# Kernel optimization log

Measured on AMD Instinct MI355X. Metric: run time of the kernel, lower is better.

The kernel has to match this reference:

```python
import jax, jax.numpy as jnp
import numpy as np

EMB = 64
D = 2 * EMB          # 128, feature dim of R / hidden of attention MLP
B, L = 128, 4096     # batch, sequence length
N_ITER = 50          # bisection iterations (entmax_bisect default)


def entmax_bisect(X, alpha, n_iter=N_ITER):
    """alpha-entmax via bisection over the last axis. X: [B, L], alpha: [B, 1] (>1)."""
    am1 = alpha - 1.0
    Xs = X * am1
    d = X.shape[-1]
    inv = 1.0 / am1
    max_val = jnp.max(Xs, axis=-1, keepdims=True)
    tau_lo0 = max_val - 1.0                       # gp(1, alpha) = 1
    tau_hi = max_val - (1.0 / d) ** am1           # gp(1/d, alpha)

    def p(tau):
        return jnp.clip(Xs - tau, 0.0, None) ** inv

    f_lo = jnp.sum(p(tau_lo0), axis=-1, keepdims=True) - 1.0

    def body(i, carry):
        tau_lo, dm, _ = carry
        dm = dm * 0.5
        tau_m = tau_lo + dm
        f_m = jnp.sum(p(tau_m), axis=-1, keepdims=True) - 1.0
        tau_lo = jnp.where(f_m * f_lo >= 0, tau_m, tau_lo)
        return (tau_lo, dm, tau_m)

    _, _, tau_m = jax.lax.fori_loop(0, n_iter, body, (tau_lo0, tau_hi - tau_lo0, tau_lo0))
    p_m = p(tau_m)
    return p_m / jnp.sum(p_m, axis=-1, keepdims=True)  # ensure_sum_one


def setup_inputs() -> dict:
    key = jax.random.key(0)
    ks = jax.random.split(key, 9)
    s = 1.0 / np.sqrt(D)
    R = jax.random.normal(ks[0], (B, L, D), dtype=jnp.float32)
    alpha = 1.25 + 0.5 * jax.random.uniform(ks[1], (B, 1), dtype=jnp.float32)  # in (1.25, 1.75)
    target = jax.random.normal(ks[2], (B, 1, D), dtype=jnp.float32)
    Wr1 = s * jax.random.normal(ks[3], (D, D), dtype=jnp.float32)      # Linear(2E, 2E), no bias
    Wr2 = s * jax.random.normal(ks[4], (D, EMB), dtype=jnp.float32)    # Linear(E, 2E) (shape-fixed), no bias
    Wr3 = s * jax.random.normal(ks[5], (1, D), dtype=jnp.float32)      # Linear(2E, 1), no bias
    bias_r = s * jax.random.normal(ks[6], (D,), dtype=jnp.float32)
    Wf_w = s * jax.random.normal(ks[7], (EMB, D), dtype=jnp.float32)   # Linear(2E, E)
    Wf_b = s * jax.random.normal(ks[8], (EMB,), dtype=jnp.float32)
    return {"R": R, "alpha": alpha, "target": target, "Wr1": Wr1, "Wr2": Wr2,
            "Wr3": Wr3, "bias_r": bias_r, "Wf_w": Wf_w, "Wf_b": Wf_b}


def reference(R, alpha, target, Wr1, Wr2, Wr3, bias_r, Wf_w, Wf_b):
    # q = Wf(target): [B, 1, E]
    q = jnp.einsum('btd,ed->bte', target, Wf_w) + Wf_b
    # additive attention score: Wr3 @ relu(Wr1 k + Wr2 q + b): [B, L]
    h = jax.nn.relu(jnp.einsum('bld,ed->ble', R, Wr1)
                    + jnp.einsum('bte,de->btd', q, Wr2)
                    + bias_r)
    scores = jnp.einsum('bld,d->bl', h, Wr3[0])
    # entmax sparsification over the sequence axis
    a = entmax_bisect(scores, alpha)
    # weighted sum of v = R: [B, D]
    res = jnp.einsum('bl,bld->bd', a, R)
    res = jax.nn.selu(res)
    res = res / jnp.linalg.norm(res, axis=-1, keepdims=True)
    return res
```

## Files before the change

kernel.cpp:

```cpp
#include <hip/hip_runtime.h>
#include <hip/hip_bf16.h>

#define B_ 128
#define L_ 4096
#define D_ 128
#define E_ 64

typedef __attribute__((ext_vector_type(8))) short short8;
typedef __attribute__((ext_vector_type(4))) float floatx4;

static __device__ __forceinline__ unsigned short f2bf(float x) {
  __hip_bfloat16 h = __float2bfloat16(x);
  union { __hip_bfloat16 h; unsigned short u; } c; c.h = h; return c.u;
}
static __device__ __forceinline__ float bf2f(unsigned short u) {
  union { unsigned short u; __hip_bfloat16 h; } c; c.u = u; return __bfloat162float(c.h);
}

__global__ __launch_bounds__(256) void prep(
    const float* __restrict__ Wr1, unsigned short* __restrict__ hi,
    unsigned short* __restrict__ lo, const float* __restrict__ target,
    const float* __restrict__ Wr2, const float* __restrict__ bias_r,
    const float* __restrict__ Wf_w, const float* __restrict__ Wf_b,
    float* __restrict__ cvec) {
  if (blockIdx.x < 64) {
    int t = blockIdx.x * 256 + threadIdx.x;
    int j = t & 7, lane = (t >> 3) & 63, ks = (t >> 9) & 3, nt = t >> 11;
    int e = nt * 16 + (lane & 15);
    int d = ks * 32 + (lane >> 4) * 8 + j;
    float x = Wr1[e * D_ + d];
    unsigned short h = f2bf(x);
    hi[t] = h;
    lo[t] = f2bf(x - bf2f(h));
  } else {
    const int sub = threadIdx.x >> 7;
    const int t = threadIdx.x & 127;
    const int b = (blockIdx.x - 64) * 2 + sub;
    __shared__ float tg[2][D_];
    __shared__ float q[2][E_];
    tg[sub][t] = target[b * D_ + t];
    __syncthreads();
    if (t < E_) {
      float s = Wf_b[t];
      #pragma unroll 8
      for (int d = 0; d < D_; ++d) s += tg[sub][d] * Wf_w[t * D_ + d];
      q[sub][t] = s;
    }
    __syncthreads();
    float s = bias_r[t];
    #pragma unroll 8
    for (int e = 0; e < E_; ++e) s += q[sub][e] * Wr2[t * E_ + e];
    cvec[b * D_ + t] = s;
  }
}

__global__ __launch_bounds__(256, 2) void pass_b(
    const float* __restrict__ R, const unsigned short* __restrict__ Whi,
    const unsigned short* __restrict__ Wlo, const float* __restrict__ cvec,
    const float* __restrict__ Wr3, float* __restrict__ scores) {
  __shared__ __align__(16) unsigned short sAhi[16384];
  __shared__ __align__(16) unsigned short sAlo[16384];
  const int b = blockIdx.x >> 5;
  const int lt = blockIdx.x & 31;
  const int t = threadIdx.x;
  const int wave = t >> 6, lane = t & 63;
  const int col = lane & 15, quad = lane >> 4;

  const float* Rbase = R + ((size_t)b * L_ + (size_t)lt * 128) * D_;
  #pragma unroll
  for (int i = 0; i < 8; ++i) {
    const int mt = wave * 2 + (i >> 2);
    const int ks = i & 3;
    const int row = mt * 16 + (lane & 15);
    const int c0 = ks * 32 + (lane >> 4) * 8;
    const float4* p = (const float4*)(Rbase + (size_t)row * D_ + c0);
    float4 v0 = p[0], v1 = p[1];
    float vv[8] = {v0.x, v0.y, v0.z, v0.w, v1.x, v1.y, v1.z, v1.w};
    union { unsigned short u[8]; short8 v; } H, Lo;
    #pragma unroll
    for (int j = 0; j < 8; ++j) {
      unsigned short h = f2bf(vv[j]);
      H.u[j] = h;
      Lo.u[j] = f2bf(vv[j] - bf2f(h));
    }
    const int base = ((mt * 4 + ks) * 64 + lane) * 8;
    *(short8*)(sAhi + base) = H.v;
    *(short8*)(sAlo + base) = Lo.v;
  }

  short8 bh[2][4], bl[2][4];
  #pragma unroll
  for (int n = 0; n < 2; ++n)
    #pragma unroll
    for (int ks = 0; ks < 4; ++ks) {
      int off = (((wave * 2 + n) * 4 + ks) * 64 + lane) * 8;
      bh[n][ks] = *(const short8*)(Whi + off);
      bl[n][ks] = *(const short8*)(Wlo + off);
    }

  floatx4 acc[8][2];
  #pragma unroll
  for (int mt = 0; mt < 8; ++mt)
    #pragma unroll
    for (int n = 0; n < 2; ++n) acc[mt][n] = (floatx4){0.f, 0.f, 0.f, 0.f};

  __syncthreads();

  #pragma unroll
  for (int mt = 0; mt < 8; ++mt) {
    #pragma unroll
    for (int ks = 0; ks < 4; ++ks) {
      int ai = ((mt * 4 + ks) * 64 + lane) * 8;
      short8 ah = *(const short8*)(sAhi + ai);
      short8 al = *(const short8*)(sAlo + ai);
      #pragma unroll
      for (int n = 0; n < 2; ++n) {
        acc[mt][n] = __builtin_amdgcn_mfma_f32_16x16x32_bf16(ah, bh[n][ks], acc[mt][n], 0, 0, 0);
        acc[mt][n] = __builtin_amdgcn_mfma_f32_16x16x32_bf16(al, bh[n][ks], acc[mt][n], 0, 0, 0);
        acc[mt][n] = __builtin_amdgcn_mfma_f32_16x16x32_bf16(ah, bl[n][ks], acc[mt][n], 0, 0, 0);
      }
    }
  }

  float w3[2], cb[2];
  #pragma unroll
  for (int n = 0; n < 2; ++n) {
    int e = (wave * 2 + n) * 16 + col;
    w3[n] = Wr3[e];
    cb[n] = cvec[b * D_ + e];
  }
  float part[8][4];
  #pragma unroll
  for (int mt = 0; mt < 8; ++mt)
    #pragma unroll
    for (int r = 0; r < 4; ++r) {
      float s = 0.f;
      #pragma unroll
      for (int n = 0; n < 2; ++n)
        s += w3[n] * fmaxf(acc[mt][n][r] + cb[n], 0.f);
      s += __shfl_xor(s, 1, 64);
      s += __shfl_xor(s, 2, 64);
      s += __shfl_xor(s, 4, 64);
      s += __shfl_xor(s, 8, 64);
      part[mt][r] = s;
    }
  __syncthreads();
  float* red = (float*)sAhi;
  if (col == 0) {
    #pragma unroll
    for (int mt = 0; mt < 8; ++mt)
      #pragma unroll
      for (int r = 0; r < 4; ++r)
        red[wave * 128 + mt * 16 + quad * 4 + r] = part[mt][r];
  }
  __syncthreads();
  if (t < 128) {
    float s = (red[t] + red[128 + t]) + (red[256 + t] + red[384 + t]);
    scores[(size_t)b * L_ + lt * 128 + t] = s;
  }
}

__global__ __launch_bounds__(512) void pass_cd(
    const float* __restrict__ scores, const float* __restrict__ alpha,
    const float* __restrict__ R, float* __restrict__ out) {
  const int b = blockIdx.x, t = threadIdx.x;
  const int wave = t >> 6, lane = t & 63;
  __shared__ float sX[L_];
  __shared__ unsigned short sI[L_];
  __shared__ float sW[L_];
  __shared__ unsigned short sJ[L_];
  __shared__ float ppart[512];
  __shared__ float sred[2][8];
  __shared__ int scnt, smcnt;
  const float am1 = alpha[b] - 1.0f;
  const float inv = 1.0f / am1;
  const float* S = scores + (size_t)b * L_;
  float Xs[8];
  #pragma unroll
  for (int i = 0; i < 8; ++i) Xs[i] = S[i * 512 + t] * am1;
  if (t == 0) { scnt = 0; smcnt = 0; }

  float mx = Xs[0];
  #pragma unroll
  for (int i = 1; i < 8; ++i) mx = fmaxf(mx, Xs[i]);
  #pragma unroll
  for (int m = 32; m >= 1; m >>= 1) mx = fmaxf(mx, __shfl_xor(mx, m, 64));
  if (lane == 0) sred[0][wave] = mx;
  __syncthreads();
  mx = sred[0][0];
  #pragma unroll
  for (int w = 1; w < 8; ++w) mx = fmaxf(mx, sred[0][w]);

  const float tau_lo0 = mx - 1.0f;
  #pragma unroll
  for (int i = 0; i < 8; ++i) {
    if (Xs[i] > tau_lo0) {
      int pos = atomicAdd(&scnt, 1);
      sX[pos] = Xs[i];
      sI[pos] = (unsigned short)(i * 512 + t);
    }
  }
  __syncthreads();
  const int n = scnt;

  float tau_lo = tau_lo0;
  float dm = (mx - exp2f(-12.0f * am1)) - tau_lo;

  int pc = 1;
  auto sumP = [&](float tau) -> float {
    const int par = pc & 1;
    ++pc;
    float s = 0.f;
    for (int k = t; k < n; k += 512) {
      float u = sX[k] - tau;
      if (u > 0.f) s += exp2f(inv * __log2f(u));
    }
    #pragma unroll
    for (int m = 32; m >= 1; m >>= 1) s += __shfl_xor(s, m, 64);
    if (lane == 0) sred[par][wave] = s;
    __syncthreads();
    float r = sred[par][0];
    #pragma unroll
    for (int w = 1; w < 8; ++w) r += sred[par][w];
    return r;
  };

  const float f_lo = sumP(tau_lo) - 1.0f;
  float tau_m = tau_lo;
  for (int it = 0; it < 40; ++it) {
    dm *= 0.5f;
    tau_m = tau_lo + dm;
    float f_m = sumP(tau_m) - 1.0f;
    if (f_m * f_lo >= 0.f) tau_lo = tau_m;
  }

  float s = 0.f;
  for (int k = t; k < n; k += 512) {
    float u = sX[k] - tau_m;
    if (u > 0.f) {
      float p = exp2f(inv * __log2f(u));
      s += p;
      int pos = atomicAdd(&smcnt, 1);
      sJ[pos] = sI[k];
      sW[pos] = p;
    }
  }
  {
    const int par = pc & 1;
    ++pc;
    #pragma unroll
    for (int m = 32; m >= 1; m >>= 1) s += __shfl_xor(s, m, 64);
    if (lane == 0) sred[par][wave] = s;
    __syncthreads();
    s = sred[par][0];
    #pragma unroll
    for (int w = 1; w < 8; ++w) s += sred[par][w];
  }
  const int ns = smcnt;
  const float rs = 1.0f / s;

  const float* Rb = R + (size_t)b * L_ * D_;
  const int g = t >> 7, c = t & 127;
  float acc = 0.f;
  int k = g;
  for (; k + 4 < ns; k += 8) {
    int i0 = sJ[k], i1 = sJ[k + 4];
    float w0 = sW[k], w1 = sW[k + 4];
    acc += w0 * Rb[(size_t)i0 * D_ + c] + w1 * Rb[(size_t)i1 * D_ + c];
  }
  for (; k < ns; k += 4) acc += sW[k] * Rb[(size_t)sJ[k] * D_ + c];
  __syncthreads();
  ppart[t] = acc;
  __syncthreads();
  float r = 0.f;
  if (t < 128) {
    float a2 = ((ppart[t] + ppart[t + 128]) + (ppart[t + 256] + ppart[t + 384])) * rs;
    const float sc = 1.0507009873554805f, al = 1.6732632423543772f;
    r = a2 > 0.f ? sc * a2 : sc * al * (expf(a2) - 1.0f);
  }
  float q = r * r;
  #pragma unroll
  for (int m = 32; m >= 1; m >>= 1) q += __shfl_xor(q, m, 64);
  if (lane == 0) sred[0][wave] = q;
  __syncthreads();
  if (t < 128) {
    float nrm = sqrtf(sred[0][0] + sred[0][1]);
    out[b * D_ + t] = r / nrm;
  }
}

extern "C" void kernel_launch(void* const* d_in, const int* in_sizes, int n_in,
                              void* d_out, int out_size, void* d_ws, size_t ws_size,
                              hipStream_t stream) {
  const float* R      = (const float*)d_in[0];
  const float* alpha  = (const float*)d_in[1];
  const float* target = (const float*)d_in[2];
  const float* Wr1    = (const float*)d_in[3];
  const float* Wr2    = (const float*)d_in[4];
  const float* Wr3    = (const float*)d_in[5];
  const float* bias_r = (const float*)d_in[6];
  const float* Wf_w   = (const float*)d_in[7];
  const float* Wf_b   = (const float*)d_in[8];
  float* out = (float*)d_out;

  char* ws = (char*)d_ws;
  float* cvec          = (float*)ws;
  unsigned short* whi  = (unsigned short*)(ws + 65536);
  unsigned short* wlo  = (unsigned short*)(ws + 98304);
  float* scores        = (float*)(ws + 131072);

  hipLaunchKernelGGL(prep, dim3(128), dim3(256), 0, stream,
                     Wr1, whi, wlo, target, Wr2, bias_r, Wf_w, Wf_b, cvec);
  hipLaunchKernelGGL(pass_b, dim3(B_ * 32), dim3(256), 0, stream,
                     R, whi, wlo, cvec, Wr3, scores);
  hipLaunchKernelGGL(pass_cd, dim3(B_), dim3(512), 0, stream,
                     scores, alpha, R, out);
}
```

Measured before the change: 468.3 us.

## Fuse prep, scoring and entmax into one kernel with last-block-done reduction

Merges the three kernels into one launch. Each block converts Wr1 to hi/lo bf16 on the fly and computes the per-batch query bias vector itself. The last of the 32 blocks per batch, detected with an atomic counter and threadfence, then runs the entmax bisection and weighted sum using 256 threads and reused shared memory. This removes launch gaps and intermediate round trips, but the tail phase now runs with half as many threads per batch and the per-block weight conversion and MLP work is repeated.

```diff
diff --git a/kernel.cpp b/kernel.cpp
--- a/kernel.cpp
+++ b/kernel.cpp
@@ -17,62 +17,36 @@
   union { unsigned short u; __hip_bfloat16 h; } c; c.u = u; return __bfloat162float(c.h);
 }
 
-__global__ __launch_bounds__(256) void prep(
-    const float* __restrict__ Wr1, unsigned short* __restrict__ hi,
-    unsigned short* __restrict__ lo, const float* __restrict__ target,
-    const float* __restrict__ Wr2, const float* __restrict__ bias_r,
-    const float* __restrict__ Wf_w, const float* __restrict__ Wf_b,
-    float* __restrict__ cvec) {
-  if (blockIdx.x < 64) {
-    int t = blockIdx.x * 256 + threadIdx.x;
-    int j = t & 7, lane = (t >> 3) & 63, ks = (t >> 9) & 3, nt = t >> 11;
-    int e = nt * 16 + (lane & 15);
-    int d = ks * 32 + (lane >> 4) * 8 + j;
-    float x = Wr1[e * D_ + d];
-    unsigned short h = f2bf(x);
-    hi[t] = h;
-    lo[t] = f2bf(x - bf2f(h));
-  } else {
-    const int sub = threadIdx.x >> 7;
-    const int t = threadIdx.x & 127;
-    const int b = (blockIdx.x - 64) * 2 + sub;
-    __shared__ float tg[2][D_];
-    __shared__ float q[2][E_];
-    tg[sub][t] = target[b * D_ + t];
-    __syncthreads();
-    if (t < E_) {
-      float s = Wf_b[t];
-      #pragma unroll 8
-      for (int d = 0; d < D_; ++d) s += tg[sub][d] * Wf_w[t * D_ + d];
-      q[sub][t] = s;
-    }
-    __syncthreads();
-    float s = bias_r[t];
-    #pragma unroll 8
-    for (int e = 0; e < E_; ++e) s += q[sub][e] * Wr2[t * E_ + e];
-    cvec[b * D_ + t] = s;
-  }
-}
-
-__global__ __launch_bounds__(256, 2) void pass_b(
-    const float* __restrict__ R, const unsigned short* __restrict__ Whi,
-    const unsigned short* __restrict__ Wlo, const float* __restrict__ cvec,
-    const float* __restrict__ Wr3, float* __restrict__ scores) {
+__global__ __launch_bounds__(256, 2) void fused(
+    const float* __restrict__ R, const float* __restrict__ alpha,
+    const float* __restrict__ target, const float* __restrict__ Wr1,
+    const float* __restrict__ Wr2, const float* __restrict__ Wr3,
+    const float* __restrict__ bias_r, const float* __restrict__ Wf_w,
+    const float* __restrict__ Wf_b, float* __restrict__ scores,
+    int* __restrict__ cnt, float* __restrict__ out) {
   __shared__ __align__(16) unsigned short sAhi[16384];
   __shared__ __align__(16) unsigned short sAlo[16384];
+  __shared__ float tg[D_];
+  __shared__ float qv[E_];
+  __shared__ float scvec[D_];
+  __shared__ float sred[2][4];
+  __shared__ int sflag, scnt, smcnt;
+
   const int b = blockIdx.x >> 5;
   const int lt = blockIdx.x & 31;
   const int t = threadIdx.x;
   const int wave = t >> 6, lane = t & 63;
   const int col = lane & 15, quad = lane >> 4;
 
+  if (t < D_) tg[t] = target[b * D_ + t];
+
   const float* Rbase = R + ((size_t)b * L_ + (size_t)lt * 128) * D_;
   #pragma unroll
   for (int i = 0; i < 8; ++i) {
     const int mt = wave * 2 + (i >> 2);
     const int ks = i & 3;
-    const int row = mt * 16 + (lane & 15);
-    const int c0 = ks * 32 + (lane >> 4) * 8;
+    const int row = mt * 16 + col;
+    const int c0 = ks * 32 + quad * 8;
     const float4* p = (const float4*)(Rbase + (size_t)row * D_ + c0);
     float4 v0 = p[0], v1 = p[1];
     float vv[8] = {v0.x, v0.y, v0.z, v0.w, v1.x, v1.y, v1.z, v1.w};
@@ -93,9 +67,20 @@
   for (int n = 0; n < 2; ++n)
     #pragma unroll
     for (int ks = 0; ks < 4; ++ks) {
-      int off = (((wave * 2 + n) * 4 + ks) * 64 + lane) * 8;
-      bh[n][ks] = *(const short8*)(Whi + off);
-      bl[n][ks] = *(const short8*)(Wlo + off);
+      const int e = (wave * 2 + n) * 16 + col;
+      const int c0 = ks * 32 + quad * 8;
+      const float4* p = (const float4*)(Wr1 + e * D_ + c0);
+      float4 v0 = p[0], v1 = p[1];
+      float vv[8] = {v0.x, v0.y, v0.z, v0.w, v1.x, v1.y, v1.z, v1.w};
+      union { unsigned short u[8]; short8 v; } H, Lo;
+      #pragma unroll
+      for (int j = 0; j < 8; ++j) {
+        unsigned short h = f2bf(vv[j]);
+        H.u[j] = h;
+        Lo.u[j] = f2bf(vv[j] - bf2f(h));
+      }
+      bh[n][ks] = H.v;
+      bl[n][ks] = Lo.v;
     }
 
   floatx4 acc[8][2];
@@ -106,11 +91,25 @@
 
   __syncthreads();
 
+  if (t < E_) {
+    float s = Wf_b[t];
+    #pragma unroll 8
+    for (int d = 0; d < D_; ++d) s += tg[d] * Wf_w[t * D_ + d];
+    qv[t] = s;
+  }
+  __syncthreads();
+  if (t < D_) {
+    float s = bias_r[t];
+    #pragma unroll 8
+    for (int e = 0; e < E_; ++e) s += qv[e] * Wr2[t * E_ + e];
+    scvec[t] = s;
+  }
+
   #pragma unroll
   for (int mt = 0; mt < 8; ++mt) {
     #pragma unroll
     for (int ks = 0; ks < 4; ++ks) {
-      int ai = ((mt * 4 + ks) * 64 + lane) * 8;
+      const int ai = ((mt * 4 + ks) * 64 + lane) * 8;
       short8 ah = *(const short8*)(sAhi + ai);
       short8 al = *(const short8*)(sAlo + ai);
       #pragma unroll
@@ -122,12 +121,14 @@
     }
   }
 
+  __syncthreads();
+
   float w3[2], cb[2];
   #pragma unroll
   for (int n = 0; n < 2; ++n) {
-    int e = (wave * 2 + n) * 16 + col;
+    const int e = (wave * 2 + n) * 16 + col;
     w3[n] = Wr3[e];
-    cb[n] = cvec[b * D_ + e];
+    cb[n] = scvec[e];
   }
   float part[8][4];
   #pragma unroll
@@ -144,7 +145,6 @@
       s += __shfl_xor(s, 8, 64);
       part[mt][r] = s;
     }
-  __syncthreads();
   float* red = (float*)sAhi;
   if (col == 0) {
     #pragma unroll
@@ -158,46 +158,46 @@
     float s = (red[t] + red[128 + t]) + (red[256 + t] + red[384 + t]);
     scores[(size_t)b * L_ + lt * 128 + t] = s;
   }
-}
-
-__global__ __launch_bounds__(512) void pass_cd(
-    const float* __restrict__ scores, const float* __restrict__ alpha,
-    const float* __restrict__ R, float* __restrict__ out) {
-  const int b = blockIdx.x, t = threadIdx.x;
-  const int wave = t >> 6, lane = t & 63;
-  __shared__ float sX[L_];
-  __shared__ unsigned short sI[L_];
-  __shared__ float sW[L_];
-  __shared__ unsigned short sJ[L_];
-  __shared__ float ppart[512];
-  __shared__ float sred[2][8];
-  __shared__ int scnt, smcnt;
+
+  __syncthreads();
+  if (t == 0) {
+    __threadfence();
+    sflag = atomicAdd(&cnt[b], 1);
+  }
+  __syncthreads();
+  if (sflag != 31) return;
+  __threadfence();
+
+  float* sX = (float*)sAhi;
+  float* sW = (float*)sAhi + 4096;
+  unsigned short* sI = sAlo;
+  unsigned short* sJ = sAlo + 4096;
+  float* ppart = (float*)(sAlo + 8192);
+
   const float am1 = alpha[b] - 1.0f;
   const float inv = 1.0f / am1;
   const float* S = scores + (size_t)b * L_;
-  float Xs[8];
-  #pragma unroll
-  for (int i = 0; i < 8; ++i) Xs[i] = S[i * 512 + t] * am1;
+  float Xs[16];
+  #pragma unroll
+  for (int i = 0; i < 16; ++i) Xs[i] = S[i * 256 + t] * am1;
   if (t == 0) { scnt = 0; smcnt = 0; }
 
   float mx = Xs[0];
   #pragma unroll
-  for (int i = 1; i < 8; ++i) mx = fmaxf(mx, Xs[i]);
+  for (int i = 1; i < 16; ++i) mx = fmaxf(mx, Xs[i]);
   #pragma unroll
   for (int m = 32; m >= 1; m >>= 1) mx = fmaxf(mx, __shfl_xor(mx, m, 64));
   if (lane == 0) sred[0][wave] = mx;
   __syncthreads();
-  mx = sred[0][0];
-  #pragma unroll
-  for (int w = 1; w < 8; ++w) mx = fmaxf(mx, sred[0][w]);
+  mx = fmaxf(fmaxf(sred[0][0], sred[0][1]), fmaxf(sred[0][2], sred[0][3]));
 
   const float tau_lo0 = mx - 1.0f;
   #pragma unroll
-  for (int i = 0; i < 8; ++i) {
+  for (int i = 0; i < 16; ++i) {
     if (Xs[i] > tau_lo0) {
       int pos = atomicAdd(&scnt, 1);
       sX[pos] = Xs[i];
-      sI[pos] = (unsigned short)(i * 512 + t);
+      sI[pos] = (unsigned short)(i * 256 + t);
     }
   }
   __syncthreads();
@@ -211,7 +211,7 @@
     const int par = pc & 1;
     ++pc;
     float s = 0.f;
-    for (int k = t; k < n; k += 512) {
+    for (int k = t; k < n; k += 256) {
       float u = sX[k] - tau;
       if (u > 0.f) s += exp2f(inv * __log2f(u));
     }
@@ -219,10 +219,7 @@
     for (int m = 32; m >= 1; m >>= 1) s += __shfl_xor(s, m, 64);
     if (lane == 0) sred[par][wave] = s;
     __syncthreads();
-    float r = sred[par][0];
-    #pragma unroll
-    for (int w = 1; w < 8; ++w) r += sred[par][w];
-    return r;
+    return (sred[par][0] + sred[par][1]) + (sred[par][2] + sred[par][3]);
   };
 
   const float f_lo = sumP(tau_lo) - 1.0f;
@@ -235,7 +232,7 @@
   }
 
   float s = 0.f;
-  for (int k = t; k < n; k += 512) {
+  for (int k = t; k < n; k += 256) {
     float u = sX[k] - tau_m;
     if (u > 0.f) {
       float p = exp2f(inv * __log2f(u));
@@ -252,39 +249,38 @@
     for (int m = 32; m >= 1; m >>= 1) s += __shfl_xor(s, m, 64);
     if (lane == 0) sred[par][wave] = s;
     __syncthreads();
-    s = sred[par][0];
-    #pragma unroll
-    for (int w = 1; w < 8; ++w) s += sred[par][w];
+    s = (sred[par][0] + sred[par][1]) + (sred[par][2] + sred[par][3]);
   }
   const int ns = smcnt;
   const float rs = 1.0f / s;
 
   const float* Rb = R + (size_t)b * L_ * D_;
   const int g = t >> 7, c = t & 127;
-  float acc = 0.f;
+  float a0 = 0.f;
   int k = g;
-  for (; k + 4 < ns; k += 8) {
-    int i0 = sJ[k], i1 = sJ[k + 4];
-    float w0 = sW[k], w1 = sW[k + 4];
-    acc += w0 * Rb[(size_t)i0 * D_ + c] + w1 * Rb[(size_t)i1 * D_ + c];
-  }
-  for (; k < ns; k += 4) acc += sW[k] * Rb[(size_t)sJ[k] * D_ + c];
-  __syncthreads();
-  ppart[t] = acc;
+  for (; k + 6 < ns; k += 8) {
+    int i0 = sJ[k], i1 = sJ[k + 2], i2 = sJ[k + 4], i3 = sJ[k + 6];
+    float w0 = sW[k], w1 = sW[k + 2], w2 = sW[k + 4], w3v = sW[k + 6];
+    a0 += w0 * Rb[(size_t)i0 * D_ + c] + w1 * Rb[(size_t)i1 * D_ + c]
+        + w2 * Rb[(size_t)i2 * D_ + c] + w3v * Rb[(size_t)i3 * D_ + c];
+  }
+  for (; k < ns; k += 2) a0 += sW[k] * Rb[(size_t)sJ[k] * D_ + c];
+  __syncthreads();
+  ppart[t] = a0;
   __syncthreads();
   float r = 0.f;
   if (t < 128) {
-    float a2 = ((ppart[t] + ppart[t + 128]) + (ppart[t + 256] + ppart[t + 384])) * rs;
+    float a2 = (ppart[t] + ppart[t + 128]) * rs;
     const float sc = 1.0507009873554805f, al = 1.6732632423543772f;
     r = a2 > 0.f ? sc * a2 : sc * al * (expf(a2) - 1.0f);
   }
-  float q = r * r;
-  #pragma unroll
-  for (int m = 32; m >= 1; m >>= 1) q += __shfl_xor(q, m, 64);
-  if (lane == 0) sred[0][wave] = q;
+  float qq = r * r;
+  #pragma unroll
+  for (int m = 32; m >= 1; m >>= 1) qq += __shfl_xor(qq, m, 64);
+  if (lane == 0) sred[0][wave] = qq;
   __syncthreads();
   if (t < 128) {
-    float nrm = sqrtf(sred[0][0] + sred[0][1]);
+    float nrm = sqrtf((sred[0][0] + sred[0][1]) + (sred[0][2] + sred[0][3]));
     out[b * D_ + t] = r / nrm;
   }
 }
@@ -304,15 +300,11 @@
   float* out = (float*)d_out;
 
   char* ws = (char*)d_ws;
-  float* cvec          = (float*)ws;
-  unsigned short* whi  = (unsigned short*)(ws + 65536);
-  unsigned short* wlo  = (unsigned short*)(ws + 98304);
-  float* scores        = (float*)(ws + 131072);
-
-  hipLaunchKernelGGL(prep, dim3(128), dim3(256), 0, stream,
-                     Wr1, whi, wlo, target, Wr2, bias_r, Wf_w, Wf_b, cvec);
-  hipLaunchKernelGGL(pass_b, dim3(B_ * 32), dim3(256), 0, stream,
-                     R, whi, wlo, cvec, Wr3, scores);
-  hipLaunchKernelGGL(pass_cd, dim3(B_), dim3(512), 0, stream,
-                     scores, alpha, R, out);
+  float* scores = (float*)ws;
+  int*   cnt    = (int*)(ws + 2097152);
+
+  hipMemsetAsync(cnt, 0, B_ * sizeof(int), stream);
+  hipLaunchKernelGGL(fused, dim3(B_ * 32), dim3(256), 0, stream,
+                     R, alpha, target, Wr1, Wr2, Wr3, bias_r, Wf_w, Wf_b,
+                     scores, cnt, out);
 }
```

Result: slower. 854.0 us (+82.4%).
